# Kernel optimization log

Measured on AMD Instinct MI355X. Metric: run time of the kernel, lower is better.

The kernel has to match this reference:

```python
import jax, jax.numpy as jnp
import numpy as np

HIDDEN = 1024
HEADS = 16
HEAD_DIM = HIDDEN // HEADS  # 64
ROPE_DIM = 64
ROPE_BASE = 10000.0
B, T = 2, 2048


def setup_inputs() -> dict:
    key = jax.random.key(0)
    k1, k2, k3, k4, k5, k6 = jax.random.split(key, 6)
    x = jax.random.normal(k1, (B, T, HIDDEN), dtype=jnp.float32)
    input_ids = jax.random.randint(k2, (B, T), 0, 32000)
    # torch Linear weights: [out_features, in_features]
    qkv_w = jax.random.normal(k3, (3 * HIDDEN, HIDDEN), dtype=jnp.float32) * (1.0 / np.sqrt(HIDDEN))
    qkv_b = jnp.zeros((3 * HIDDEN,), dtype=jnp.float32)
    out_w = jax.random.normal(k4, (HIDDEN, HIDDEN), dtype=jnp.float32) * (1.0 / np.sqrt(HIDDEN))
    out_b = jnp.zeros((HIDDEN,), dtype=jnp.float32)
    global_idx = jnp.array([0, 1, 2], dtype=jnp.int64)  # special_tokens values
    return {"x": x, "input_ids": input_ids, "qkv_w": qkv_w, "qkv_b": qkv_b,
            "out_w": out_w, "out_b": out_b, "global_idx": global_idx}


def _rope_cos_sin(t, offset=0):
    inv_freq = 1.0 / (ROPE_BASE ** (jnp.arange(0, ROPE_DIM, 2, dtype=jnp.float32) / ROPE_DIM))  # [ROPE_DIM/2]
    pos = jnp.arange(offset, offset + t, dtype=jnp.float32)
    freqs = pos[:, None] * inv_freq[None, :]  # [T, ROPE_DIM/2]
    return jnp.cos(freqs)[None, None], jnp.sin(freqs)[None, None]  # [1,1,T,ROPE_DIM/2]


def _apply_rotary(x, cos, sin):
    x_rot, x_pass = x[..., :ROPE_DIM], x[..., ROPE_DIM:]
    half = ROPE_DIM // 2
    x1, x2 = x_rot[..., :half], x_rot[..., half:]
    return jnp.concatenate([x1 * cos - x2 * sin, x1 * sin + x2 * cos, x_pass], axis=-1)


def reference(x, input_ids, qkv_w, qkv_b, out_w, out_b, global_idx):
    b, t, _ = x.shape
    qkv = x @ qkv_w.T + qkv_b  # [B,T,3*HIDDEN]
    q, k, v = jnp.split(qkv, 3, axis=-1)
    # -> [B, H, T, Dh]
    reshape = lambda z: z.reshape(b, t, HEADS, HEAD_DIM).transpose(0, 2, 1, 3)
    q, k, v = reshape(q), reshape(k), reshape(v)
    cos, sin = _rope_cos_sin(t)
    q = _apply_rotary(q, cos, sin)
    k = _apply_rotary(k, cos, sin)
    # causal + global-query mask
    causal = jnp.tril(jnp.ones((t, t), dtype=bool))[None, None]  # [1,1,T,T]
    global_mask = jnp.isin(input_ids, global_idx)  # [B,T]
    allow = causal | global_mask[:, None, :, None]  # [B,1,T,T]
    scale = jnp.sqrt(jnp.float32(HEAD_DIM))
    logits = jnp.einsum('bhqd,bhkd->bhqk', q, k) / scale
    neg = -jnp.finfo(logits.dtype).max
    logits = jnp.where(allow, logits, neg)
    attn = jax.nn.softmax(logits, axis=-1)
    out = jnp.einsum('bhqk,bhkd->bhqd', attn, v)  # [B,H,T,Dh]
    out = out.transpose(0, 2, 1, 3).reshape(b, t, HEADS * HEAD_DIM)
    return out @ out_w.T + out_b
```

## Files before the change

### kernel.cpp

```cpp
#include <hip/hip_runtime.h>
#include <hip/hip_bf16.h>
#include <math.h>

typedef __bf16 bf16;
typedef __bf16 bf16x4 __attribute__((ext_vector_type(4)));
typedef __bf16 bf16x8 __attribute__((ext_vector_type(8)));
typedef float floatx4 __attribute__((ext_vector_type(4)));

#define HIDDEN 1024
#define NHEADS 16
#define HDIM 64
#define TSEQ 2048
#define NBATCH 2
#define MTOT (NBATCH * TSEQ)

__device__ inline void glds16(bf16* lds, const bf16* g)
{
  __builtin_amdgcn_global_load_lds(
      (const __attribute__((address_space(1))) unsigned int*)g,
      (__attribute__((address_space(3))) unsigned int*)lds, 16, 0, 0);
}

__global__ __launch_bounds__(256) void prep_kernel(
    const float* __restrict__ x, bf16* __restrict__ xb,
    const float* __restrict__ qkv_w, bf16* __restrict__ qkv_wb,
    float2* __restrict__ rope)
{
  const int bid = blockIdx.x;
  if (bid >= 3584) {
    const int e0 = ((bid - 3584) * 256 + threadIdx.x) * 4;
    const int t = e0 >> 5;
    const int d2 = e0 & 31;
#pragma unroll
    for (int j = 0; j < 4; j++) {
      const float inv = exp2f((float)(d2 + j) * -0.41524100f);
      float s, c;
      sincosf((float)t * inv, &s, &c);
      rope[e0 + j] = make_float2(c, s);
    }
    return;
  }
  const float* src = (bid < 2048) ? x : qkv_w;
  bf16* dst = (bid < 2048) ? xb : qkv_wb;
  const int i = (((bid < 2048) ? bid : bid - 2048) * 256 + threadIdx.x) * 8;
  const floatx4 u = *(const floatx4*)(src + i);
  const floatx4 v = *(const floatx4*)(src + i + 4);
  bf16x8 r;
#pragma unroll
  for (int j = 0; j < 4; j++) { r[j] = (bf16)u[j]; r[4 + j] = (bf16)v[j]; }
  *(bf16x8*)(dst + i) = r;
}

__global__ __launch_bounds__(256) void cvt_f32_bf16(
    const float* __restrict__ src, bf16* __restrict__ dst, int n)
{
  const int i = (blockIdx.x * 256 + threadIdx.x) * 8;
  if (i >= n) return;
  const floatx4 u = *(const floatx4*)(src + i);
  const floatx4 v = *(const floatx4*)(src + i + 4);
  bf16x8 r;
#pragma unroll
  for (int j = 0; j < 4; j++) { r[j] = (bf16)u[j]; r[4 + j] = (bf16)v[j]; }
  *(bf16x8*)(dst + i) = r;
}

__global__ __launch_bounds__(256) void gemm_qkv(
    const bf16* __restrict__ A, const bf16* __restrict__ W,
    const float* __restrict__ bias, const float2* __restrict__ rope,
    bf16* __restrict__ Qb, bf16* __restrict__ Kb, bf16* __restrict__ Vt,
    int M, int N, int K)
{
  __shared__ bf16 As[128 * 32];
  __shared__ bf16 Bs[128 * 32];

  const int tid  = threadIdx.x;
  const int lane = tid & 63;
  const int wv   = tid >> 6;
  const int quad = lane >> 4;
  const int l16  = lane & 15;
  const int m0 = blockIdx.y * 128;
  const int n0 = blockIdx.x * 128;
  const int wm = (wv >> 1) * 64;
  const int wn = (wv & 1) * 64;

  const int srow = lane >> 2;
  const int scol = (lane & 3) * 8;

  floatx4 acc[4][4];
#pragma unroll
  for (int i = 0; i < 4; i++)
#pragma unroll
    for (int j = 0; j < 4; j++) acc[i][j] = (floatx4){0.f, 0.f, 0.f, 0.f};

  for (int k0 = 0; k0 < K; k0 += 32) {
    __syncthreads();
    const bf16* ga = A + (size_t)(m0 + wv * 32 + srow) * K + k0 + scol;
    glds16(As + (wv * 32) * 32, ga);
    glds16(As + (wv * 32 + 16) * 32, ga + (size_t)16 * K);
    const bf16* gb = W + (size_t)(n0 + wv * 32 + srow) * K + k0 + scol;
    glds16(Bs + (wv * 32) * 32, gb);
    glds16(Bs + (wv * 32 + 16) * 32, gb + (size_t)16 * K);
    __syncthreads();

    bf16x8 af[4], bfr[4];
#pragma unroll
    for (int i = 0; i < 4; i++)
      af[i] = *(const bf16x8*)(As + (wm + i * 16 + l16) * 32 + quad * 8);
#pragma unroll
    for (int j = 0; j < 4; j++)
      bfr[j] = *(const bf16x8*)(Bs + (wn + j * 16 + l16) * 32 + quad * 8);
#pragma unroll
    for (int i = 0; i < 4; i++)
#pragma unroll
      for (int j = 0; j < 4; j++)
        acc[i][j] = __builtin_amdgcn_mfma_f32_16x16x32_bf16(af[i], bfr[j], acc[i][j], 0, 0, 0);
  }

  const int sect = n0 >> 10;
  const int hw   = ((n0 & 1023) + wn) >> 6;

  float bs[4];
#pragma unroll
  for (int j = 0; j < 4; j++) bs[j] = bias[n0 + wn + j * 16 + l16];

  if (sect < 2) {
    bf16* dst = sect ? Kb : Qb;
#pragma unroll
    for (int i = 0; i < 4; i++) {
      const int gmBase = m0 + wm + i * 16 + quad * 4;
#pragma unroll
      for (int r = 0; r < 4; r++) {
        const int gm = gmBase + r;
        const int b_ = gm >> 11, t = gm & 2047;
        const size_t rowbase = ((size_t)(b_ * NHEADS + hw) * TSEQ + t) * HDIM;
        const float2 cs0 = rope[t * 32 + l16];
        const float2 cs1 = rope[t * 32 + 16 + l16];
        const float x1a = acc[i][0][r] + bs[0];
        const float x2a = acc[i][2][r] + bs[2];
        const float x1b = acc[i][1][r] + bs[1];
        const float x2b = acc[i][3][r] + bs[3];
        dst[rowbase + l16]      = (bf16)(x1a * cs0.x - x2a * cs0.y);
        dst[rowbase + 32 + l16] = (bf16)(x1a * cs0.y + x2a * cs0.x);
        dst[rowbase + 16 + l16] = (bf16)(x1b * cs1.x - x2b * cs1.y);
        dst[rowbase + 48 + l16] = (bf16)(x1b * cs1.y + x2b * cs1.x);
      }
    }
  } else {
#pragma unroll
    for (int j = 0; j < 4; j++) {
      const int d = j * 16 + l16;
#pragma unroll
      for (int i = 0; i < 4; i++) {
        const int gmBase = m0 + wm + i * 16 + quad * 4;
        const int b_ = gmBase >> 11, t0 = gmBase & 2047;
        bf16x4 vv;
#pragma unroll
        for (int r = 0; r < 4; r++) vv[r] = (bf16)(acc[i][j][r] + bs[j]);
        *(bf16x4*)(Vt + ((size_t)((b_ * NHEADS + hw) * HDIM + d)) * TSEQ + t0) = vv;
      }
    }
  }
}

__global__ __launch_bounds__(256) void gemm_out(
    const bf16* __restrict__ A, const bf16* __restrict__ W,
    const float* __restrict__ bias, float* __restrict__ C,
    int M, int N, int K)
{
  __shared__ bf16 As[128 * 32];
  __shared__ bf16 Bs[128 * 32];

  const int tid  = threadIdx.x;
  const int lane = tid & 63;
  const int wv   = tid >> 6;
  const int quad = lane >> 4;
  const int l16  = lane & 15;
  const int m0 = blockIdx.y * 128;
  const int n0 = blockIdx.x * 128;
  const int wm = (wv >> 1) * 64;
  const int wn = (wv & 1) * 64;

  const int srow = lane >> 2;
  const int scol = (lane & 3) * 8;

  floatx4 acc[4][4];
#pragma unroll
  for (int i = 0; i < 4; i++)
#pragma unroll
    for (int j = 0; j < 4; j++) acc[i][j] = (floatx4){0.f, 0.f, 0.f, 0.f};

  for (int k0 = 0; k0 < K; k0 += 32) {
    __syncthreads();
    const bf16* ga = A + (size_t)(m0 + wv * 32 + srow) * K + k0 + scol;
    glds16(As + (wv * 32) * 32, ga);
    glds16(As + (wv * 32 + 16) * 32, ga + (size_t)16 * K);
    const bf16* gb = W + (size_t)(n0 + wv * 32 + srow) * K + k0 + scol;
    glds16(Bs + (wv * 32) * 32, gb);
    glds16(Bs + (wv * 32 + 16) * 32, gb + (size_t)16 * K);
    __syncthreads();

    bf16x8 af[4], bfr[4];
#pragma unroll
    for (int i = 0; i < 4; i++)
      af[i] = *(const bf16x8*)(As + (wm + i * 16 + l16) * 32 + quad * 8);
#pragma unroll
    for (int j = 0; j < 4; j++)
      bfr[j] = *(const bf16x8*)(Bs + (wn + j * 16 + l16) * 32 + quad * 8);
#pragma unroll
    for (int i = 0; i < 4; i++)
#pragma unroll
      for (int j = 0; j < 4; j++)
        acc[i][j] = __builtin_amdgcn_mfma_f32_16x16x32_bf16(af[i], bfr[j], acc[i][j], 0, 0, 0);
  }

#pragma unroll
  for (int i = 0; i < 4; i++) {
    const int gmBase = m0 + wm + i * 16 + quad * 4;
#pragma unroll
    for (int j = 0; j < 4; j++) {
      const int gn = n0 + wn + j * 16 + l16;
      const float bsv = bias[gn];
#pragma unroll
      for (int r = 0; r < 4; r++)
        C[(size_t)(gmBase + r) * N + gn] = acc[i][j][r] + bsv;
    }
  }
}

__device__ inline int swz(int g) { return (g & ~7) | ((g ^ (g >> 3) ^ (g >> 6)) & 7); }

__global__ __launch_bounds__(256) void attn_kernel(
    const bf16* __restrict__ Q, const bf16* __restrict__ K,
    const bf16* __restrict__ Vt, bf16* __restrict__ O,
    const int* __restrict__ ids, const int* __restrict__ gidx)
{
  __shared__ bf16 Ks[4096];
  __shared__ bf16 Vs[4096];
  __shared__ int flags[4];

  const int tid  = threadIdx.x;
  const int lane = tid & 63;
  const int wv   = tid >> 6;
  const int quad = lane >> 4;
  const int l16  = lane & 15;

  const int xcd = blockIdx.x & 7;
  const int j   = blockIdx.x >> 3;
  const int bh  = xcd * 4 + (j >> 4);
  const int p   = j & 15;
  const int b  = bh >> 4;
  const int h  = bh & 15;

  const bf16* Qp = Q + (size_t)bh * TSEQ * HDIM;
  const bf16* Kp = K + (size_t)bh * TSEQ * HDIM;
  const bf16* Vp = Vt + (size_t)bh * HDIM * TSEQ;

  const int rK  = tid >> 3;
  const int dcK = tid & 7;
  const int gk = ((rK >> 2) & 1) * 128 + (dcK >> 2) * 64 +
                 ((dcK & 3) * 16 + (((rK >> 3) << 2) | (rK & 3)));
  const int kd0 = swz(gk) * 8, kd1 = swz(gk + 256) * 8;
  const int dV = tid >> 3;
  const int uV = tid & 7;
  const int gv = (uV >> 2) * 256 + (dV >> 4) * 64 + ((uV & 3) * 16 + (dV & 15));
  const int vd0 = swz(gv) * 8, vd1 = swz(gv + 128) * 8;

  const int g0v = gidx[0], g1v = gidx[1], g2v = gidx[2];

#pragma unroll
  for (int ph = 0; ph < 2; ph++) {
    const int qt = ph ? p : (31 - p);
    const int q0 = qt * 64 + wv * 16;

    const bf16x8 qf0 = *(const bf16x8*)(Qp + (size_t)(q0 + l16) * HDIM + quad * 8);
    const bf16x8 qf1 = *(const bf16x8*)(Qp + (size_t)(q0 + l16) * HDIM + 32 + quad * 8);

    const int myq = q0 + l16;
    const int myid = ids[b * TSEQ + myq];
    const int gl = (myid == g0v) | (myid == g1v) | (myid == g2v);
    flags[wv] = __any(gl);
    __syncthreads();
    const int anyg = flags[0] | flags[1] | flags[2] | flags[3];
    const int kmax = anyg ? TSEQ : (qt * 64 + 64);

    float lsum = 0.f;
    floatx4 o[4];
#pragma unroll
    for (int nt = 0; nt < 4; nt++) o[nt] = (floatx4){0.f, 0.f, 0.f, 0.f};

    bf16x8 kA = *(const bf16x8*)(Kp + tid * 8);
    bf16x8 kB = *(const bf16x8*)(Kp + 2048 + tid * 8);
    bf16x8 vA = *(const bf16x8*)(Vp + (size_t)dV * TSEQ + uV * 8);
    bf16x8 vB = *(const bf16x8*)(Vp + (size_t)(dV + 32) * TSEQ + uV * 8);

    for (int k0 = 0; k0 < kmax; k0 += 64) {
      __syncthreads();
      *(bf16x8*)(Ks + kd0) = kA;
      *(bf16x8*)(Ks + kd1) = kB;
      *(bf16x8*)(Vs + vd0) = vA;
      *(bf16x8*)(Vs + vd1) = vB;
      __syncthreads();

      if (k0 + 64 < kmax) {
        const bf16* kc = Kp + (size_t)(k0 + 64) * HDIM;
        kA = *(const bf16x8*)(kc + tid * 8);
        kB = *(const bf16x8*)(kc + 2048 + tid * 8);
        vA = *(const bf16x8*)(Vp + (size_t)dV * TSEQ + k0 + 64 + uV * 8);
        vB = *(const bf16x8*)(Vp + (size_t)(dV + 32) * TSEQ + k0 + 64 + uV * 8);
      }

#pragma unroll
      for (int g = 0; g < 2; g++) {
        const int kb = k0 + g * 32;
        const int rb = g * 256 + lane;
        const bf16x8 a00 = *(const bf16x8*)(Ks + swz(rb) * 8);
        const bf16x8 a01 = *(const bf16x8*)(Ks + swz(rb + 64) * 8);
        const bf16x8 a10 = *(const bf16x8*)(Ks + swz(rb + 128) * 8);
        const bf16x8 a11 = *(const bf16x8*)(Ks + swz(rb + 192) * 8);
        floatx4 s0 = (floatx4){0.f, 0.f, 0.f, 0.f};
        floatx4 s1 = (floatx4){0.f, 0.f, 0.f, 0.f};
        s0 = __builtin_amdgcn_mfma_f32_16x16x32_bf16(a00, qf0, s0, 0, 0, 0);
        s0 = __builtin_amdgcn_mfma_f32_16x16x32_bf16(a01, qf1, s0, 0, 0, 0);
        s1 = __builtin_amdgcn_mfma_f32_16x16x32_bf16(a10, qf0, s1, 0, 0, 0);
        s1 = __builtin_amdgcn_mfma_f32_16x16x32_bf16(a11, qf1, s1, 0, 0, 0);

        bf16x8 pf;
#pragma unroll
        for (int r = 0; r < 4; r++) {
          const int key0 = kb + quad * 8 + r;
          const int key1 = key0 + 4;
          const float p0 = (gl || key0 <= myq) ? __expf(s0[r] * 0.125f) : 0.f;
          const float p1 = (gl || key1 <= myq) ? __expf(s1[r] * 0.125f) : 0.f;
          lsum += p0 + p1;
          pf[r]     = (bf16)p0;
          pf[4 + r] = (bf16)p1;
        }

#pragma unroll
        for (int nt = 0; nt < 4; nt++) {
          const bf16x8 vf = *(const bf16x8*)(Vs + swz(g * 256 + nt * 64 + lane) * 8);
          o[nt] = __builtin_amdgcn_mfma_f32_16x16x32_bf16(pf, vf, o[nt], 0, 0, 0);
        }
      }
    }

    lsum += __shfl_xor(lsum, 16);
    lsum += __shfl_xor(lsum, 32);

#pragma unroll
    for (int r = 0; r < 4; r++) {
      const float inv = 1.0f / __shfl(lsum, quad * 4 + r);
      const int q = q0 + quad * 4 + r;
      const size_t rowoff = ((size_t)b * TSEQ + q) * HIDDEN + h * HDIM;
#pragma unroll
      for (int nt = 0; nt < 4; nt++)
        O[rowoff + nt * 16 + l16] = (bf16)(o[nt][r] * inv);
    }
  }
}

extern "C" void kernel_launch(void* const* d_in, const int* in_sizes, int n_in,
                              void* d_out, int out_size, void* d_ws, size_t ws_size,
                              hipStream_t stream)
{
  const float* x     = (const float*)d_in[0];
  const int*   ids   = (const int*)d_in[1];
  const float* qkv_w = (const float*)d_in[2];
  const float* qkv_b = (const float*)d_in[3];
  const float* out_w = (const float*)d_in[4];
  const float* out_b = (const float*)d_in[5];
  const int*   gidx  = (const int*)d_in[6];
  float* out = (float*)d_out;

  char* ws = (char*)d_ws;
  bf16* Q      = (bf16*)(ws);
  bf16* Kb     = (bf16*)(ws + (size_t)(8u << 20));
  bf16* Vt     = (bf16*)(ws + (size_t)(16u << 20));
  bf16* slot24 = (bf16*)(ws + (size_t)(24u << 20));
  bf16* xb     = slot24;
  bf16* O      = slot24;
  bf16* out_wb = (bf16*)(ws + (size_t)(16u << 20));
  bf16* qkv_wb = (bf16*)d_out;
  float2* rope = (float2*)((char*)d_out + (size_t)(6u << 20));

  prep_kernel<<<3648, 256, 0, stream>>>(x, xb, qkv_w, qkv_wb, rope);
  gemm_qkv<<<dim3(3072 / 128, MTOT / 128), 256, 0, stream>>>(
      xb, qkv_wb, qkv_b, rope, Q, Kb, Vt, MTOT, 3 * HIDDEN, HIDDEN);
  attn_kernel<<<512, 256, 0, stream>>>(Q, Kb, Vt, O, ids, gidx);
  cvt_f32_bf16<<<512, 256, 0, stream>>>(out_w, out_wb, HIDDEN * HIDDEN);
  gemm_out<<<dim3(HIDDEN / 128, MTOT / 128), 256, 0, stream>>>(
      O, out_wb, out_b, out, MTOT, HIDDEN, HIDDEN);
}
```

Baseline: 213.5 us.

## Triple-buffer GEMM LDS tiles with async prefetch and swizzled layout

Both projection GEMMs now use a three-stage LDS ring buffer. Tiles are prefetched two steps ahead via global_load_lds, with a vmcnt wait and a single barrier per K step, replacing the old two-barrier load-then-compute loop. The LDS column offsets are also XOR-swizzled on both the write and read sides to reduce bank conflicts on fragment reads. The cost is three times the LDS per block, which may lower occupancy, plus reliance on hand-written waitcnt ordering.

```diff
diff --git a/kernel.cpp b/kernel.cpp
--- a/kernel.cpp
+++ b/kernel.cpp
@@ -64,57 +64,76 @@
   *(bf16x8*)(dst + i) = r;
 }
 
+
+#define GEMM_PROLOGUE()                                                     \
+  const int tid  = threadIdx.x;                                             \
+  const int lane = tid & 63;                                                \
+  const int wv   = tid >> 6;                                                \
+  const int quad = lane >> 4;                                               \
+  const int l16  = lane & 15;                                               \
+  const int m0 = blockIdx.y * 128;                                          \
+  const int n0 = blockIdx.x * 128;                                          \
+  const int wm = (wv >> 1) * 64;                                            \
+  const int wn = (wv & 1) * 64;                                             \
+  const int srow = lane >> 2;                                               \
+  const int scol = ((lane & 3) ^ ((lane >> 3) & 3)) * 8;   \
+  const int qsw  = (quad ^ ((l16 >> 1) & 3)) * 8;         \
+  const bf16* ga0 = A + (size_t)(m0 + wv * 32 + srow) * K + scol;           \
+  const bf16* gb0 = W + (size_t)(n0 + wv * 32 + srow) * K + scol;           \
+  floatx4 acc[4][4];                                                        \
+  _Pragma("unroll") for (int i = 0; i < 4; i++)                             \
+      _Pragma("unroll") for (int j = 0; j < 4; j++)                         \
+          acc[i][j] = (floatx4){0.f, 0.f, 0.f, 0.f};
+
+#define STAGE(buf, kk)                                                      \
+  glds16(&As[buf][(wv * 32) * 32], ga0 + (kk));                             \
+  glds16(&As[buf][(wv * 32 + 16) * 32], ga0 + (size_t)16 * K + (kk));       \
+  glds16(&Bs[buf][(wv * 32) * 32], gb0 + (kk));                             \
+  glds16(&Bs[buf][(wv * 32 + 16) * 32], gb0 + (size_t)16 * K + (kk));
+
+#define COMPUTE(buf)                                                        \
+  {                                                                         \
+    bf16x8 af[4], bfr[4];                                                   \
+    _Pragma("unroll") for (int i = 0; i < 4; i++)                           \
+        af[i] = *(const bf16x8*)(&As[buf][(wm + i * 16 + l16) * 32 + qsw]); \
+    _Pragma("unroll") for (int j = 0; j < 4; j++)                           \
+        bfr[j] = *(const bf16x8*)(&Bs[buf][(wn + j * 16 + l16) * 32 + qsw]);\
+    _Pragma("unroll") for (int i = 0; i < 4; i++)                           \
+        _Pragma("unroll") for (int j = 0; j < 4; j++)                       \
+            acc[i][j] = __builtin_amdgcn_mfma_f32_16x16x32_bf16(            \
+                af[i], bfr[j], acc[i][j], 0, 0, 0);                         \
+  }
+
+#define GEMM_MAIN_LOOP()                                                    \
+  STAGE(0, 0);                                                              \
+  STAGE(1, 32);                                                             \
+  int cur = 0;                                                              \
+  const int nsteps = K / 32;                                                \
+  _Pragma("unroll 1") for (int t = 0; t < nsteps - 1; t++) {                \
+    asm volatile("s_waitcnt vmcnt(4)" ::: "memory");                        \
+    __builtin_amdgcn_s_barrier();                                           \
+    if (t + 2 < nsteps) {                                                   \
+      const int nb = (cur >= 1) ? cur - 1 : cur + 2;                        \
+      STAGE(nb, (t + 2) * 32);                                              \
+    }                                                                       \
+    COMPUTE(cur);                                                           \
+    cur = (cur == 2) ? 0 : cur + 1;                                         \
+  }                                                                         \
+  asm volatile("s_waitcnt vmcnt(0)" ::: "memory");                          \
+  __builtin_amdgcn_s_barrier();                                             \
+  COMPUTE(cur);
+
 __global__ __launch_bounds__(256) void gemm_qkv(
     const bf16* __restrict__ A, const bf16* __restrict__ W,
     const float* __restrict__ bias, const float2* __restrict__ rope,
     bf16* __restrict__ Qb, bf16* __restrict__ Kb, bf16* __restrict__ Vt,
     int M, int N, int K)
 {
-  __shared__ bf16 As[128 * 32];
-  __shared__ bf16 Bs[128 * 32];
-
-  const int tid  = threadIdx.x;
-  const int lane = tid & 63;
-  const int wv   = tid >> 6;
-  const int quad = lane >> 4;
-  const int l16  = lane & 15;
-  const int m0 = blockIdx.y * 128;
-  const int n0 = blockIdx.x * 128;
-  const int wm = (wv >> 1) * 64;
-  const int wn = (wv & 1) * 64;
-
-  const int srow = lane >> 2;
-  const int scol = (lane & 3) * 8;
-
-  floatx4 acc[4][4];
-#pragma unroll
-  for (int i = 0; i < 4; i++)
-#pragma unroll
-    for (int j = 0; j < 4; j++) acc[i][j] = (floatx4){0.f, 0.f, 0.f, 0.f};
-
-  for (int k0 = 0; k0 < K; k0 += 32) {
-    __syncthreads();
-    const bf16* ga = A + (size_t)(m0 + wv * 32 + srow) * K + k0 + scol;
-    glds16(As + (wv * 32) * 32, ga);
-    glds16(As + (wv * 32 + 16) * 32, ga + (size_t)16 * K);
-    const bf16* gb = W + (size_t)(n0 + wv * 32 + srow) * K + k0 + scol;
-    glds16(Bs + (wv * 32) * 32, gb);
-    glds16(Bs + (wv * 32 + 16) * 32, gb + (size_t)16 * K);
-    __syncthreads();
-
-    bf16x8 af[4], bfr[4];
-#pragma unroll
-    for (int i = 0; i < 4; i++)
-      af[i] = *(const bf16x8*)(As + (wm + i * 16 + l16) * 32 + quad * 8);
-#pragma unroll
-    for (int j = 0; j < 4; j++)
-      bfr[j] = *(const bf16x8*)(Bs + (wn + j * 16 + l16) * 32 + quad * 8);
-#pragma unroll
-    for (int i = 0; i < 4; i++)
-#pragma unroll
-      for (int j = 0; j < 4; j++)
-        acc[i][j] = __builtin_amdgcn_mfma_f32_16x16x32_bf16(af[i], bfr[j], acc[i][j], 0, 0, 0);
-  }
+  __shared__ bf16 As[3][128 * 32];
+  __shared__ bf16 Bs[3][128 * 32];
+
+  GEMM_PROLOGUE();
+  GEMM_MAIN_LOOP();
 
   const int sect = n0 >> 10;
   const int hw   = ((n0 & 1023) + wn) >> 6;
@@ -167,51 +186,11 @@
     const float* __restrict__ bias, float* __restrict__ C,
     int M, int N, int K)
 {
-  __shared__ bf16 As[128 * 32];
-  __shared__ bf16 Bs[128 * 32];
-
-  const int tid  = threadIdx.x;
-  const int lane = tid & 63;
-  const int wv   = tid >> 6;
-  const int quad = lane >> 4;
-  const int l16  = lane & 15;
-  const int m0 = blockIdx.y * 128;
-  const int n0 = blockIdx.x * 128;
-  const int wm = (wv >> 1) * 64;
-  const int wn = (wv & 1) * 64;
-
-  const int srow = lane >> 2;
-  const int scol = (lane & 3) * 8;
-
-  floatx4 acc[4][4];
-#pragma unroll
-  for (int i = 0; i < 4; i++)
-#pragma unroll
-    for (int j = 0; j < 4; j++) acc[i][j] = (floatx4){0.f, 0.f, 0.f, 0.f};
-
-  for (int k0 = 0; k0 < K; k0 += 32) {
-    __syncthreads();
-    const bf16* ga = A + (size_t)(m0 + wv * 32 + srow) * K + k0 + scol;
-    glds16(As + (wv * 32) * 32, ga);
-    glds16(As + (wv * 32 + 16) * 32, ga + (size_t)16 * K);
-    const bf16* gb = W + (size_t)(n0 + wv * 32 + srow) * K + k0 + scol;
-    glds16(Bs + (wv * 32) * 32, gb);
-    glds16(Bs + (wv * 32 + 16) * 32, gb + (size_t)16 * K);
-    __syncthreads();
-
-    bf16x8 af[4], bfr[4];
-#pragma unroll
-    for (int i = 0; i < 4; i++)
-      af[i] = *(const bf16x8*)(As + (wm + i * 16 + l16) * 32 + quad * 8);
-#pragma unroll
-    for (int j = 0; j < 4; j++)
-      bfr[j] = *(const bf16x8*)(Bs + (wn + j * 16 + l16) * 32 + quad * 8);
-#pragma unroll
-    for (int i = 0; i < 4; i++)
-#pragma unroll
-      for (int j = 0; j < 4; j++)
-        acc[i][j] = __builtin_amdgcn_mfma_f32_16x16x32_bf16(af[i], bfr[j], acc[i][j], 0, 0, 0);
-  }
+  __shared__ bf16 As[3][128 * 32];
+  __shared__ bf16 Bs[3][128 * 32];
+
+  GEMM_PROLOGUE();
+  GEMM_MAIN_LOOP();
 
 #pragma unroll
   for (int i = 0; i < 4; i++) {
```

Measured after the change: 203.0 us. -4.9%, faster.
